# Optimization experiments

Measured on AMD Instinct MI355X. Metric: run time of the kernel, lower is better.

The kernel has to match this reference:

```python
import jax, jax.numpy as jnp
import numpy as np

B, T, C, H, N = 2, 1024, 2048, 32, 64  # batch, seq, n_embd==dim_att, heads, head_size
EPS_GN = 64e-5  # torch GroupNorm eps=0.00064


def setup_inputs() -> dict:
    key = jax.random.key(0)
    ks = jax.random.split(key, 40)
    def rn(i, shape, s):
        return jax.random.normal(ks[i], shape, dtype=jnp.float32) * s
    return {
        'x': jax.random.normal(ks[0], (B, T, C), dtype=jnp.float32),
        'shift_state': jnp.zeros((B, C), jnp.float32),
        'wkv_state': jnp.zeros((B, H, N, N), jnp.float32),
        'time_maa_x': rn(1, (1, 1, C), 0.3),
        'time_maa_rg': rn(2, (1, 1, C), 0.3),
        'time_maa_wa': rn(3, (1, 1, C), 0.3),
        'time_maa_k': rn(4, (1, 1, C), 0.3),
        'time_maa_v': rn(5, (1, 1, C), 0.3),
        'time_maa_w1': rn(6, (C, 128), 0.02),   # D_MIX_LORA*4 = 128
        'time_maa_w2': rn(7, (4, 32, C), 0.02),
        'time_decay': rn(8, (1, 1, C), 0.5) - 4.0,
        'time_decay_w1': rn(9, (C, 64), 0.02),
        'time_decay_w2': rn(10, (64, C), 0.02),
        'time_faaaa': rn(11, (1, 1, H, N), 0.02),
        'time_aaaaa': rn(12, (1, 1, C), 0.02),
        'time_aaa_w1': rn(13, (C, 16), 0.02),
        'time_aaa_w2': rn(14, (16, C), 0.02),
        'time_kkk_w1': rn(15, (C, 16), 0.02),
        'time_kkk_w2': rn(16, (16, C), 0.02),
        'gate_w1': rn(17, (C, 128), 0.02),
        'gate_w2': rn(18, (128, C), 0.02),
        'ma_w1': rn(19, (C, 16), 0.02),
        'ma_w2': rn(20, (16, C), 0.02),
        'time_misc_a': rn(21, (1, 1, C), 0.02),
        'mk_w1': rn(22, (C, 16), 0.02),
        'mk_w2': rn(23, (16, C), 0.02),
        'time_misc_k': rn(24, (1, 1, C), 0.02),
        'Wr': rn(25, (C, C), 0.5 / np.sqrt(C)),
        'Wk': rn(26, (C, C), 0.05 / np.sqrt(C)),
        'Wv': rn(27, (C, C), 0.5 / np.sqrt(C)),
        'Wo': rn(28, (C, C), 0.5 / np.sqrt(C)),
        'ln_w': jnp.ones((C,), jnp.float32),
        'ln_b': jnp.zeros((C,), jnp.float32),
    }


def _forward(x, shift_state, wkv_state, time_maa_x, time_maa_rg, time_maa_wa,
             time_maa_k, time_maa_v, time_maa_w1, time_maa_w2, time_decay,
             time_decay_w1, time_decay_w2, time_faaaa, time_aaaaa, time_aaa_w1,
             time_aaa_w2, time_kkk_w1, time_kkk_w2, gate_w1, gate_w2, ma_w1,
             ma_w2, time_misc_a, mk_w1, mk_w2, time_misc_k, Wr, Wk, Wv, Wo,
             ln_w, ln_b):
    # token shift difference
    xx = jnp.concatenate([shift_state[:, None, :], x[:, :-1]], axis=1) - x
    xmx = x + xx * time_maa_x
    m = jnp.tanh(xmx @ time_maa_w1).reshape(B, T, 4, -1)   # [B,T,4,32]
    m = jnp.einsum('btfd,fdc->fbtc', m, time_maa_w2)       # [4,B,T,C]
    mrg, mwa, mkm, mv = m[0], m[1], m[2], m[3]
    xrg = x + xx * (time_maa_rg + mrg)
    xwa = x + xx * (time_maa_wa + mwa)
    xk = x + xx * (time_maa_k + mkm)
    xv = x + xx * (time_maa_v + mv)
    r = xrg @ Wr.T
    w = -jax.nn.softplus(-(time_decay + jnp.tanh(xwa @ time_decay_w1) @ time_decay_w2)) - 0.5
    k = xk @ Wk.T
    v = xv @ Wv.T
    g = jnp.tanh(xrg @ gate_w1) @ gate_w2
    kk = k + jnp.tanh(xk @ time_kkk_w1) @ time_kkk_w2
    kkh = kk.reshape(B, T, H, N)
    nrm = jnp.maximum(jnp.linalg.norm(kkh, axis=-1, keepdims=True), 1e-12)  # F.normalize
    kk = (kkh / nrm).reshape(B, T, C)
    a = jax.nn.sigmoid(time_aaaaa + xwa @ time_aaa_w1 @ time_aaa_w2)
    ma = jax.nn.sigmoid(time_misc_a + xwa @ ma_w1 @ ma_w2)
    k = k * ma + k * a * (1.0 - ma)
    mk = jax.nn.sigmoid(time_misc_k + xk @ mk_w1 @ mk_w2)
    k = k * jnp.exp(jnp.minimum(w * mk, 0.0))  # clamp(w*mk, max=0).exp()

    # RWKV-7 recurrence (fused_recurrent_rwkv7 with a=-kk, b=kk*a_gate):
    #   S_t = diag(exp(w_t)) S_{t-1} + b_t (a_t^T S_{t-1}) + k_t v_t^T,  o_t = S_t^T r_t
    def heads(t):
        return jnp.moveaxis(t.reshape(B, T, H, N), 1, 0)  # [T,B,H,N]
    rs, ksq, vs, ws = heads(r), heads(k), heads(v), heads(w)
    a_s, b_s = heads(-kk), heads(kk * a)

    def step(S, inputs):  # S: [B,H,N_key,N_val]
        r_t, k_t, v_t, w_t, a_t, b_t = inputs
        sa = jnp.einsum('bhk,bhkv->bhv', a_t, S)
        S = S * jnp.exp(w_t)[..., None] + k_t[..., None] * v_t[..., None, :] + b_t[..., None] * sa[..., None, :]
        o = jnp.einsum('bhk,bhkv->bhv', r_t, S)
        return S, o

    S_final, o = jax.lax.scan(step, wkv_state, (rs, ksq, vs, ws, a_s, b_s))
    out = jnp.moveaxis(o, 0, 1).reshape(B, T, C)

    # GroupNorm(n_head groups, eps=64e-5), biased variance per head
    y = out.reshape(B * T, H, N)
    mu = y.mean(-1, keepdims=True)
    var = ((y - mu) ** 2).mean(-1, keepdims=True)
    y = (y - mu) / jnp.sqrt(var + EPS_GN)
    y = y * ln_w.reshape(H, N) + ln_b.reshape(H, N)
    xo = y.reshape(B, T, C)

    rh = r.reshape(B, T, H, N)
    kh = k.reshape(B, T, H, N)
    vh = v.reshape(B, T, H, N)
    xo = xo + ((rh * kh * time_faaaa).sum(-1, keepdims=True) * vh).reshape(B, T, C)
    xo = (xo * g) @ Wo.T
    return xo, x[:, -1], S_final


def reference(x, shift_state, wkv_state, time_maa_x, time_maa_rg, time_maa_wa,
              time_maa_k, time_maa_v, time_maa_w1, time_maa_w2, time_decay,
              time_decay_w1, time_decay_w2, time_faaaa, time_aaaaa, time_aaa_w1,
              time_aaa_w2, time_kkk_w1, time_kkk_w2, gate_w1, gate_w2, ma_w1,
              ma_w2, time_misc_a, mk_w1, mk_w2, time_misc_k, Wr, Wk, Wv, Wo,
              ln_w, ln_b):
    return _forward(x, shift_state, wkv_state, time_maa_x, time_maa_rg, time_maa_wa,
                    time_maa_k, time_maa_v, time_maa_w1, time_maa_w2, time_decay,
                    time_decay_w1, time_decay_w2, time_faaaa, time_aaaaa, time_aaa_w1,
                    time_aaa_w2, time_kkk_w1, time_kkk_w2, gate_w1, gate_w2, ma_w1,
                    ma_w2, time_misc_a, mk_w1, mk_w2, time_misc_k, Wr, Wk, Wv, Wo,
                    ln_w, ln_b)
```

## Files before the change

### kernel.cpp

```cpp
#include <hip/hip_runtime.h>
#include <hip/hip_bf16.h>
#include <math.h>


#define B_ 2
#define T_ 1024
#define C_ 2048
#define H_ 32
#define BT_ (B_*T_)
#define BTC_ ((size_t)BT_*C_)
#define CC_ ((size_t)C_*C_)
#define KS_ 8
#define CH_ 8

typedef __bf16 bf16x8 __attribute__((ext_vector_type(8)));
typedef float f32x4 __attribute__((ext_vector_type(4)));

__device__ __forceinline__ float wave64_sum(float v){
#pragma unroll
  for (int d = 1; d < 64; d <<= 1) v += __shfl_xor(v, d, 64);
  return v;
}

__device__ __forceinline__ float dpp_add_xor1(float x){
  int j = __builtin_amdgcn_mov_dpp(__float_as_int(x), 0xB1, 0xF, 0xF, true);
  return x + __int_as_float(j);
}
__device__ __forceinline__ float dpp_add_xor2(float x){
  int j = __builtin_amdgcn_mov_dpp(__float_as_int(x), 0x4E, 0xF, 0xF, true);
  return x + __int_as_float(j);
}
__device__ __forceinline__ float dpp_add_hmir(float x){
  int j = __builtin_amdgcn_mov_dpp(__float_as_int(x), 0x141, 0xF, 0xF, true);
  return x + __int_as_float(j);
}
__device__ __forceinline__ float dpp_add_mir(float x){
  int j = __builtin_amdgcn_mov_dpp(__float_as_int(x), 0x140, 0xF, 0xF, true);
  return x + __int_as_float(j);
}

__device__ __forceinline__ float red16(float x){
  x = dpp_add_xor1(x);
  x = dpp_add_xor2(x);
  x = dpp_add_hmir(x);
  x = dpp_add_mir(x);
  return x;
}

__device__ __forceinline__ size_t bhtn_idx(int r, int c){
  return (((size_t)(r >> 10)*H_ + (c >> 6))*T_ + (r & 1023))*64 + (c & 63);
}

__device__ __forceinline__ void gload_lds16(const float* g, float* l){
  __builtin_amdgcn_global_load_lds((const __attribute__((address_space(1))) void*)g,
                                   (__attribute__((address_space(3))) void*)l, 16, 0, 0);
}
__device__ __forceinline__ void gload_lds16b(const __hip_bfloat16* g, __bf16* l){
  __builtin_amdgcn_global_load_lds((const __attribute__((address_space(1))) void*)g,
                                   (__attribute__((address_space(3))) void*)l, 16, 0, 0);
}

__global__ __launch_bounds__(256) void f2bf_kernel(const float* __restrict__ in,
                                                   __hip_bfloat16* __restrict__ out, size_t n){
  size_t i = (size_t)blockIdx.x*256 + threadIdx.x;
  if (i < n) out[i] = __float2bfloat16(in[i]);
}

__global__ __launch_bounds__(256) void shift_kernel(const float* __restrict__ x,
                                                    const float* __restrict__ shift,
                                                    const float* __restrict__ maa_x,
                                                    float* __restrict__ xx, __hip_bfloat16* __restrict__ xmx_h){
  size_t idx = (size_t)blockIdx.x*256 + threadIdx.x;
  int c = (int)(idx % C_);
  size_t bt = idx / C_;
  int t = (int)(bt % T_);
  int b = (int)(bt / T_);
  float xv = x[idx];
  float prev = (t == 0) ? shift[(size_t)b*C_ + c] : x[idx - C_];
  float d = prev - xv;
  xx[idx] = d;
  xmx_h[idx] = __float2bfloat16(xv + d * maa_x[c]);
}

__global__ __launch_bounds__(256) void tp_pack(const float* __restrict__ in, __hip_bfloat16* __restrict__ out,
                                               int Nsrc, int row_off){
  __shared__ float tile[32][33];
  const int t = threadIdx.x;
  const int k0 = blockIdx.x*32, n0 = blockIdx.y*32;
  const int tn = t & 31, tk = t >> 5;
#pragma unroll
  for (int q = 0; q < 4; q++){
    int ki = tk + 8*q;
    float v = (n0 + tn < Nsrc) ? in[(size_t)(k0+ki)*Nsrc + n0 + tn] : 0.f;
    tile[tn][ki] = v;
  }
  __syncthreads();
#pragma unroll
  for (int q = 0; q < 4; q++){
    int no = tk + 8*q;
    if (n0 + no < Nsrc)
      out[(size_t)(row_off + n0 + no)*2048 + k0 + tn] = __float2bfloat16(tile[no][tn]);
  }
}

__global__ __launch_bounds__(256) void gemm_sk(const __hip_bfloat16* __restrict__ Ah,
                                               const __hip_bfloat16* __restrict__ Bh,
                                               float* __restrict__ parts, int K, int KC){
  __shared__ __bf16 As[2][128*32];
  __shared__ __bf16 Bs[2][128*32];
  const int tid = threadIdx.x;
  const int bm = blockIdx.x*128;
  const int z = blockIdx.y;
  const int wid = tid >> 6, lane = tid & 63;
  const int wr = (wid >> 1)*64, wc = (wid & 1)*64;
  const int fr = lane & 15, kg = lane >> 4;
  const int srow = tid >> 2, sk = (tid & 3)*8;
  f32x4 acc[4][4] = {};
  const int kend = z*KC + KC;
#define SK_STAGE(kt_, b_) do{ \
    gload_lds16b(Ah + (size_t)(bm+srow)*K + (kt_) + sk,    As[b_] + wid*512); \
    gload_lds16b(Ah + (size_t)(bm+srow+64)*K + (kt_) + sk, As[b_] + wid*512 + 64*32); \
    gload_lds16b(Bh + (size_t)(srow)*K + (kt_) + sk,       Bs[b_] + wid*512); \
    gload_lds16b(Bh + (size_t)(srow+64)*K + (kt_) + sk,    Bs[b_] + wid*512 + 64*32); \
  }while(0)
  SK_STAGE(z*KC, 0);
  __builtin_amdgcn_s_waitcnt(0x3F70);
  __builtin_amdgcn_s_barrier();
  __builtin_amdgcn_sched_barrier(0);
  int buf = 0;
  for (int kt = z*KC; kt < kend; kt += 32){
    if (kt + 32 < kend) SK_STAGE(kt+32, buf^1);
    bf16x8 af[4], bfr[4];
#pragma unroll
    for (int i = 0; i < 4; i++){
      af[i]  = *(const bf16x8*)(As[buf] + (wr + i*16 + fr)*32 + kg*8);
      bfr[i] = *(const bf16x8*)(Bs[buf] + (wc + i*16 + fr)*32 + kg*8);
    }
#pragma unroll
    for (int mi = 0; mi < 4; mi++)
#pragma unroll
      for (int ni = 0; ni < 4; ni++)
        acc[mi][ni] = __builtin_amdgcn_mfma_f32_16x16x32_bf16(af[mi], bfr[ni], acc[mi][ni], 0, 0, 0);
    __builtin_amdgcn_sched_barrier(0);
    __builtin_amdgcn_s_waitcnt(0x3F70);
    __builtin_amdgcn_s_barrier();
    __builtin_amdgcn_sched_barrier(0);
    buf ^= 1;
  }
#undef SK_STAGE
  float* Cc = parts + (size_t)z*BT_*128;
  const int orow0 = bm + wr + kg*4;
  const int ocol0 = wc + fr;
#pragma unroll
  for (int mi = 0; mi < 4; mi++)
#pragma unroll
    for (int ni = 0; ni < 4; ni++)
#pragma unroll
      for (int j = 0; j < 4; j++)
        Cc[(size_t)(orow0 + mi*16 + j)*128 + ocol0 + ni*16] = acc[mi][ni][j];
}

__global__ __launch_bounds__(256) void reduce_sk(const float* __restrict__ parts, float* __restrict__ out,
                                                 int tanh_lo, int tanh_hi){
  size_t idx = (size_t)blockIdx.x*256 + threadIdx.x;
  float s = 0.f;
#pragma unroll
  for (int z = 0; z < KS_; z++) s += parts[(size_t)z*BT_*128 + idx];
  int c = (int)(idx & 127);
  if (c >= tanh_lo && c < tanh_hi) s = tanhf(s);
  out[idx] = s;
}

__global__ __launch_bounds__(256) void mm_sk_g(const float* __restrict__ A, const float* __restrict__ W,
                                               __hip_bfloat16* __restrict__ out, int K){
  const int j = blockIdx.y*256 + threadIdx.x;
  const int i0 = blockIdx.x*8;
  float acc[8] = {0,0,0,0,0,0,0,0};
  for (int k = 0; k < K; k++){
    float wv = W[(size_t)k*C_ + j];
#pragma unroll
    for (int r = 0; r < 8; r++) acc[r] += A[(size_t)(i0+r)*K + k] * wv;
  }
#pragma unroll
  for (int r = 0; r < 8; r++) out[(size_t)(i0+r)*C_ + j] = __float2bfloat16(acc[r]);
}

__global__ __launch_bounds__(256) void mix_kernel(
    const float* __restrict__ m1, const float* __restrict__ w2,
    const float* __restrict__ x, const float* __restrict__ xx,
    const float* __restrict__ maa_rg, const float* __restrict__ maa_wa,
    const float* __restrict__ maa_k, const float* __restrict__ maa_v,
    __hip_bfloat16* __restrict__ xrg_h, __hip_bfloat16* __restrict__ xwa_h,
    __hip_bfloat16* __restrict__ xk_h, __hip_bfloat16* __restrict__ xv_h)
{
  const int j = blockIdx.y*256 + threadIdx.x;
  const int i0 = blockIdx.x*8;
  float acc[4][8] = {};
#pragma unroll
  for (int f = 0; f < 4; f++){
    for (int d = 0; d < 32; d++){
      float wv = w2[((size_t)f*32 + d)*C_ + j];
#pragma unroll
      for (int r = 0; r < 8; r++)
        acc[f][r] += m1[(size_t)(i0+r)*128 + f*32 + d] * wv;
    }
  }
  float mrg_ = maa_rg[j], mwa_ = maa_wa[j], mk_ = maa_k[j], mv_ = maa_v[j];
#pragma unroll
  for (int r = 0; r < 8; r++){
    size_t idx = (size_t)(i0+r)*C_ + j;
    float xval = x[idx], xxv = xx[idx];
    xrg_h[idx] = __float2bfloat16(xval + xxv*(mrg_ + acc[0][r]));
    xwa_h[idx] = __float2bfloat16(xval + xxv*(mwa_ + acc[1][r]));
    xk_h[idx]  = __float2bfloat16(xval + xxv*(mk_  + acc[2][r]));
    xv_h[idx]  = __float2bfloat16(xval + xxv*(mv_  + acc[3][r]));
  }
}

__global__ __launch_bounds__(256) void gemm_bt(const __hip_bfloat16* __restrict__ Ah,
                                               const __hip_bfloat16* __restrict__ Bh,
                                               float* __restrict__ Cc, int M, int Nn, int K){
  __shared__ __bf16 As[2][128*32];
  __shared__ __bf16 Bs[2][128*32];
  const int tid = threadIdx.x;
  const int bm = blockIdx.x*128, bn = blockIdx.y*128;
  const int wid = tid >> 6, lane = tid & 63;
  const int wr = (wid >> 1)*64, wc = (wid & 1)*64;
  const int fr = lane & 15, kg = lane >> 4;
  const int srow = tid >> 2, sk = (tid & 3)*8;
  f32x4 acc[4][4] = {};
#define BT_STAGE(kt_, b_) do{ \
    gload_lds16b(Ah + (size_t)(bm+srow)*K + (kt_) + sk,    As[b_] + wid*512); \
    gload_lds16b(Ah + (size_t)(bm+srow+64)*K + (kt_) + sk, As[b_] + wid*512 + 64*32); \
    gload_lds16b(Bh + (size_t)(bn+srow)*K + (kt_) + sk,    Bs[b_] + wid*512); \
    gload_lds16b(Bh + (size_t)(bn+srow+64)*K + (kt_) + sk, Bs[b_] + wid*512 + 64*32); \
  }while(0)
  BT_STAGE(0, 0);
  __builtin_amdgcn_s_waitcnt(0x3F70);
  __builtin_amdgcn_s_barrier();
  __builtin_amdgcn_sched_barrier(0);
  int buf = 0;
  for (int kt = 0; kt < K; kt += 32){
    if (kt + 32 < K) BT_STAGE(kt+32, buf^1);
    bf16x8 af[4], bfr[4];
#pragma unroll
    for (int i = 0; i < 4; i++){
      af[i]  = *(const bf16x8*)(As[buf] + (wr + i*16 + fr)*32 + kg*8);
      bfr[i] = *(const bf16x8*)(Bs[buf] + (wc + i*16 + fr)*32 + kg*8);
    }
#pragma unroll
    for (int mi = 0; mi < 4; mi++)
#pragma unroll
      for (int ni = 0; ni < 4; ni++)
        acc[mi][ni] = __builtin_amdgcn_mfma_f32_16x16x32_bf16(af[mi], bfr[ni], acc[mi][ni], 0, 0, 0);
    __builtin_amdgcn_sched_barrier(0);
    __builtin_amdgcn_s_waitcnt(0x3F70);
    __builtin_amdgcn_s_barrier();
    __builtin_amdgcn_sched_barrier(0);
    buf ^= 1;
  }
#undef BT_STAGE
  const int orow0 = bm + wr + kg*4;
  const int ocol0 = bn + wc + fr;
#pragma unroll
  for (int mi = 0; mi < 4; mi++)
#pragma unroll
    for (int ni = 0; ni < 4; ni++)
#pragma unroll
      for (int j = 0; j < 4; j++)
        Cc[(size_t)(orow0 + mi*16 + j)*Nn + ocol0 + ni*16] = acc[mi][ni][j];
}

__global__ __launch_bounds__(256) void gemm_bt_T3(
    const __hip_bfloat16* __restrict__ A0, const __hip_bfloat16* __restrict__ A1,
    const __hip_bfloat16* __restrict__ A2,
    const __hip_bfloat16* __restrict__ B0, const __hip_bfloat16* __restrict__ B1,
    const __hip_bfloat16* __restrict__ B2,
    float* __restrict__ C0, float* __restrict__ C1, float* __restrict__ C2, int K)
{
  __shared__ __bf16 As[2][128*32];
  __shared__ __bf16 Bs[2][128*32];
  const int zi = blockIdx.z;
  const __hip_bfloat16* Ah = (zi == 0) ? A0 : (zi == 1) ? A1 : A2;
  const __hip_bfloat16* Bh = (zi == 0) ? B0 : (zi == 1) ? B1 : B2;
  float* Cc = (zi == 0) ? C0 : (zi == 1) ? C1 : C2;
  const int tid = threadIdx.x;
  const int bm = blockIdx.x*128, bn = blockIdx.y*128;
  const int wid = tid >> 6, lane = tid & 63;
  const int wr = (wid >> 1)*64, wc = (wid & 1)*64;
  const int fr = lane & 15, kg = lane >> 4;
  const int srow = tid >> 2, sk = (tid & 3)*8;
  f32x4 acc[4][4] = {};
#define T3_STAGE(kt_, b_) do{ \
    gload_lds16b(Ah + (size_t)(bm+srow)*K + (kt_) + sk,    As[b_] + wid*512); \
    gload_lds16b(Ah + (size_t)(bm+srow+64)*K + (kt_) + sk, As[b_] + wid*512 + 64*32); \
    gload_lds16b(Bh + (size_t)(bn+srow)*K + (kt_) + sk,    Bs[b_] + wid*512); \
    gload_lds16b(Bh + (size_t)(bn+srow+64)*K + (kt_) + sk, Bs[b_] + wid*512 + 64*32); \
  }while(0)
  T3_STAGE(0, 0);
  __builtin_amdgcn_s_waitcnt(0x3F70);
  __builtin_amdgcn_s_barrier();
  __builtin_amdgcn_sched_barrier(0);
  int buf = 0;
  for (int kt = 0; kt < K; kt += 32){
    if (kt + 32 < K) T3_STAGE(kt+32, buf^1);
    bf16x8 af[4], bfr[4];
#pragma unroll
    for (int i = 0; i < 4; i++){
      af[i]  = *(const bf16x8*)(As[buf] + (wr + i*16 + fr)*32 + kg*8);
      bfr[i] = *(const bf16x8*)(Bs[buf] + (wc + i*16 + fr)*32 + kg*8);
    }
#pragma unroll
    for (int mi = 0; mi < 4; mi++)
#pragma unroll
      for (int ni = 0; ni < 4; ni++)
        acc[mi][ni] = __builtin_amdgcn_mfma_f32_16x16x32_bf16(af[mi], bfr[ni], acc[mi][ni], 0, 0, 0);
    __builtin_amdgcn_sched_barrier(0);
    __builtin_amdgcn_s_waitcnt(0x3F70);
    __builtin_amdgcn_s_barrier();
    __builtin_amdgcn_sched_barrier(0);
    buf ^= 1;
  }
#undef T3_STAGE
  const int r0 = bm + wr + kg*4;
  const int c0 = bn + wc + fr;
#pragma unroll
  for (int mi = 0; mi < 4; mi++)
#pragma unroll
    for (int ni = 0; ni < 4; ni++)
#pragma unroll
      for (int j = 0; j < 4; j++)
        Cc[bhtn_idx(r0 + mi*16 + j, c0 + ni*16)] = acc[mi][ni][j];
}

__global__ __launch_bounds__(256) void lora2_kernel(
    const float* __restrict__ wa1, const float* __restrict__ k1c,
    const float* __restrict__ dw2, const float* __restrict__ aw2, const float* __restrict__ maw2,
    const float* __restrict__ mkw2, const float* __restrict__ kkw2,
    const float* __restrict__ td, const float* __restrict__ aaaaa,
    const float* __restrict__ misc_a, const float* __restrict__ misc_k,
    float* __restrict__ k0, float* __restrict__ a_out,
    float* __restrict__ ew_out, float* __restrict__ kk0_out)
{
  const int j = blockIdx.y*256 + threadIdx.x;
  const int i0 = blockIdx.x*8;
  float accW[8] = {}, accA[8] = {}, accMA[8] = {}, accMK[8] = {}, accKK[8] = {};
  for (int k = 0; k < 64; k++){
    float wv = dw2[(size_t)k*C_ + j];
#pragma unroll
    for (int r = 0; r < 8; r++) accW[r] += wa1[(size_t)(i0+r)*128 + k] * wv;
  }
  for (int k = 0; k < 16; k++){
    float w_a  = aw2[(size_t)k*C_ + j];
    float w_ma = maw2[(size_t)k*C_ + j];
    float w_mk = mkw2[(size_t)k*C_ + j];
    float w_kk = kkw2[(size_t)k*C_ + j];
#pragma unroll
    for (int r = 0; r < 8; r++){
      accA[r]  += wa1[(size_t)(i0+r)*128 + 64 + k] * w_a;
      accMA[r] += wa1[(size_t)(i0+r)*128 + 80 + k] * w_ma;
      accKK[r] += k1c[(size_t)(i0+r)*128 + k] * w_kk;
      accMK[r] += k1c[(size_t)(i0+r)*128 + 16 + k] * w_mk;
    }
  }
  float tdv = td[j], aav = aaaaa[j], mav = misc_a[j], mkv = misc_k[j];
#pragma unroll
  for (int r = 0; r < 8; r++){
    size_t idx = bhtn_idx(i0+r, j);
    float u  = tdv + accW[r];
    float w  = -log1pf(expf(-u)) - 0.5f;
    float a  = 1.f/(1.f + expf(-(aav + accA[r])));
    float ma = 1.f/(1.f + expf(-(mav + accMA[r])));
    float mk = 1.f/(1.f + expf(-(mkv + accMK[r])));
    float kv = k0[idx];
    kk0_out[idx] = kv + accKK[r];
    float kn = kv * (ma + a*(1.f - ma)) * expf(fminf(w*mk, 0.f));
    k0[idx] = kn;
    a_out[idx] = a;
    ew_out[idx] = expf(w);
  }
}

__global__ __launch_bounds__(256) void kknorm_kernel(float* __restrict__ kk0, float* __restrict__ a_bs){
  const size_t grp = (size_t)blockIdx.x*4 + (threadIdx.x >> 6);
  const int lane = threadIdx.x & 63;
  const size_t idx = grp*64 + lane;
  float kv = kk0[idx];
  float ss = wave64_sum(kv*kv);
  float nrm = fmaxf(sqrtf(ss), 1e-12f);
  float kkn = kv / nrm;
  kk0[idx] = kkn;
  a_bs[idx] = kkn * a_bs[idx];
}

__global__ __launch_bounds__(64, 1) void rec_kernel(
    const float* __restrict__ rr, const float* __restrict__ kx,
    const float* __restrict__ vx, const float* __restrict__ ew,
    const float* __restrict__ kkv, const float* __restrict__ bsv,
    const float* __restrict__ s0, float* __restrict__ o, float* __restrict__ sT)
{
  __shared__ __align__(16) float lds[2][6][CH_*64];
  const int g = blockIdx.x;
  const int bh = g & 63;
  const int vg = g >> 6;
  const int b = bh >> 5, h = bh & 31;
  const int lane = threadIdx.x;
  const int cf = lane >> 4;
  const int kq = lane & 15;
  const int k0 = kq*4;
  const int v = vg*4 + cf;

  float S0, S1, S2, S3;
  {
    const float* p = s0 + ((size_t)bh*64 + k0)*64 + v;
    S0 = p[0]; S1 = p[64]; S2 = p[128]; S3 = p[192];
  }

  const size_t sb = (size_t)bh*T_*64;
  const float* g0 = kkv + sb;
  const float* g1 = ew  + sb;
  const float* g2 = kx  + sb;
  const float* g3 = bsv + sb;
  const float* g4 = rr  + sb;
  const float* g5 = vx  + sb;
  float* ob = o + (size_t)b*T_*C_ + h*64 + v;

#define STAGE(c, buf) do{ \
    const size_t co_ = (size_t)(c)*(CH_*64) + lane*4; \
    _Pragma("unroll") \
    for (int j_ = 0; j_ < 2; j_++){ \
      gload_lds16(g0 + co_ + j_*256, &lds[buf][0][j_*256]); \
      gload_lds16(g1 + co_ + j_*256, &lds[buf][1][j_*256]); \
      gload_lds16(g2 + co_ + j_*256, &lds[buf][2][j_*256]); \
      gload_lds16(g3 + co_ + j_*256, &lds[buf][3][j_*256]); \
      gload_lds16(g4 + co_ + j_*256, &lds[buf][4][j_*256]); \
      gload_lds16(g5 + co_ + j_*256, &lds[buf][5][j_*256]); \
    } }while(0)

  STAGE(0, 0);
  const int NCH = T_/CH_;
  for (int c = 0; c < NCH; c++){
    const int cn = (c+1 < NCH) ? c+1 : c;
    STAGE(cn, (c+1)&1);
    __builtin_amdgcn_s_waitcnt(0x0F7C);
    __builtin_amdgcn_sched_barrier(0);
    const int buf = c & 1;
#pragma unroll
    for (int s = 0; s < CH_; s++){
      const int so = s*64 + k0;
      const float4 A  = *(const float4*)(&lds[buf][0][so]);
      const float4 E  = *(const float4*)(&lds[buf][1][so]);
      const float4 Kk = *(const float4*)(&lds[buf][2][so]);
      const float4 Bv = *(const float4*)(&lds[buf][3][so]);
      const float4 R  = *(const float4*)(&lds[buf][4][so]);
      const float vt  = lds[buf][5][s*64 + v];
      float p = (A.x*S0 + A.y*S1) + (A.z*S2 + A.w*S3);
      p = red16(p);
      S0 = S0*E.x + Kk.x*vt - Bv.x*p;
      S1 = S1*E.y + Kk.y*vt - Bv.y*p;
      S2 = S2*E.z + Kk.z*vt - Bv.z*p;
      S3 = S3*E.w + Kk.w*vt - Bv.w*p;
      float op = (R.x*S0 + R.y*S1) + (R.z*S2 + R.w*S3);
      op = red16(op);
      if (kq == 0)
        ob[(size_t)(c*CH_ + s)*C_] = op;
    }
  }
#undef STAGE
  float* pT = sT + ((size_t)bh*64 + k0)*64 + v;
  pT[0] = S0; pT[64] = S1; pT[128] = S2; pT[192] = S3;
}

__global__ __launch_bounds__(256) void post_kernel(
    const float* __restrict__ o, const float* __restrict__ r, const float* __restrict__ k,
    const float* __restrict__ v, const __hip_bfloat16* __restrict__ g,
    const float* __restrict__ lnw, const float* __restrict__ lnb,
    const float* __restrict__ faaaa, __hip_bfloat16* __restrict__ z_h)
{
  const size_t grp = (size_t)blockIdx.x*4 + (threadIdx.x >> 6);
  const int lane = threadIdx.x & 63;
  const int h = (int)(grp & (H_-1));
  const int bt = (int)(grp >> 5);
  const size_t idx  = grp*64 + lane;
  const size_t idx2 = (((size_t)(bt >> 10)*H_ + h)*T_ + (bt & 1023))*64 + lane;
  const int ci = h*64 + lane;
  float y = o[idx];
  float mu = wave64_sum(y) * (1.f/64.f);
  float d = y - mu;
  float var = wave64_sum(d*d) * (1.f/64.f);
  float yn = d * rsqrtf(var + 64e-5f) * lnw[ci] + lnb[ci];
  float s = wave64_sum(r[idx2]*k[idx2]*faaaa[ci]);
  float xo = yn + s*v[idx2];
  z_h[idx] = __float2bfloat16(xo * __bfloat162float(g[idx]));
}

__global__ __launch_bounds__(256) void lastx_kernel(const float* __restrict__ x, float* __restrict__ out1){
  int idx = blockIdx.x*256 + threadIdx.x;
  int b = idx / C_, c = idx % C_;
  out1[idx] = x[((size_t)b*T_ + (T_-1))*C_ + c];
}

extern "C" void kernel_launch(void* const* d_in, const int* in_sizes, int n_in,
                              void* d_out, int out_size, void* d_ws, size_t ws_size,
                              hipStream_t stream){
  (void)in_sizes; (void)n_in; (void)out_size;
  const float* x      = (const float*)d_in[0];
  const float* shift  = (const float*)d_in[1];
  const float* wkv0   = (const float*)d_in[2];
  const float* maa_x  = (const float*)d_in[3];
  const float* maa_rg = (const float*)d_in[4];
  const float* maa_wa = (const float*)d_in[5];
  const float* maa_k  = (const float*)d_in[6];
  const float* maa_v  = (const float*)d_in[7];
  const float* maa_w1 = (const float*)d_in[8];
  const float* maa_w2 = (const float*)d_in[9];
  const float* tdecay = (const float*)d_in[10];
  const float* dw1    = (const float*)d_in[11];
  const float* dw2    = (const float*)d_in[12];
  const float* faaaa  = (const float*)d_in[13];
  const float* aaaaa  = (const float*)d_in[14];
  const float* aw1    = (const float*)d_in[15];
  const float* aw2    = (const float*)d_in[16];
  const float* kkw1   = (const float*)d_in[17];
  const float* kkw2   = (const float*)d_in[18];
  const float* gw1    = (const float*)d_in[19];
  const float* gw2    = (const float*)d_in[20];
  const float* maw1   = (const float*)d_in[21];
  const float* maw2   = (const float*)d_in[22];
  const float* misc_a = (const float*)d_in[23];
  const float* mkw1   = (const float*)d_in[24];
  const float* mkw2   = (const float*)d_in[25];
  const float* misc_k = (const float*)d_in[26];
  const float* Wr     = (const float*)d_in[27];
  const float* Wk     = (const float*)d_in[28];
  const float* Wv     = (const float*)d_in[29];
  const float* Wo     = (const float*)d_in[30];
  const float* lnw    = (const float*)d_in[31];
  const float* lnb    = (const float*)d_in[32];

  float* out0 = (float*)d_out;
  float* out1 = out0 + BTC_;
  float* outS = out1 + (size_t)B_*C_;

  const size_t NEEDED = (6*BTC_ + (size_t)3*BT_*128)*4 + 5*CC_*2 + (size_t)4*128*2048*2;
  if (ws_size < NEEDED) return;

  float* ws = (float*)d_ws;
  float* rbuf  = ws;
  float* kbuf  = ws + 1*BTC_;
  float* vbuf  = ws + 2*BTC_;
  float* abuf  = ws + 3*BTC_;
  float* ewbuf = ws + 4*BTC_;
  float* kkbuf = ws + 5*BTC_;
  float* xx    = abuf;
  float* wa1   = ws + 6*BTC_;
  float* g1f   = wa1 + (size_t)BT_*128;
  float* k1c   = g1f + (size_t)BT_*128;
  float* parts = rbuf;
  float* m1f   = vbuf;
  __hip_bfloat16* hb = (__hip_bfloat16*)(k1c + (size_t)BT_*128);
  __hip_bfloat16* xrg_h = hb;
  __hip_bfloat16* xwa_h = hb + 1*CC_;
  __hip_bfloat16* xk_h  = hb + 2*CC_;
  __hip_bfloat16* xv_h  = hb + 3*CC_;
  __hip_bfloat16* Wb    = hb + 4*CC_;
  __hip_bfloat16* WtB   = hb + 5*CC_;
  __hip_bfloat16* Wt_m  = WtB;
  __hip_bfloat16* Wt_wa = WtB + (size_t)128*2048;
  __hip_bfloat16* Wt_g  = WtB + (size_t)2*128*2048;
  __hip_bfloat16* Wt_k  = WtB + (size_t)3*128*2048;
  __hip_bfloat16* xmx_h = xv_h;
  __hip_bfloat16* g_h   = xwa_h;
  __hip_bfloat16* z_h   = xv_h;
  __hip_bfloat16* Wk_h  = (__hip_bfloat16*)ewbuf;
  __hip_bfloat16* Wv_h  = (__hip_bfloat16*)kkbuf;

  dim3 blk(256);
  const int KC = C_/KS_;

  hipMemsetAsync(WtB, 0, (size_t)4*128*2048*2, stream);
  tp_pack<<<dim3(64,4), blk, 0, stream>>>(maa_w1, Wt_m, 128, 0);
  tp_pack<<<dim3(64,2), blk, 0, stream>>>(dw1,  Wt_wa, 64, 0);
  tp_pack<<<dim3(64,1), blk, 0, stream>>>(aw1,  Wt_wa, 16, 64);
  tp_pack<<<dim3(64,1), blk, 0, stream>>>(maw1, Wt_wa, 16, 80);
  tp_pack<<<dim3(64,4), blk, 0, stream>>>(gw1,  Wt_g, 128, 0);
  tp_pack<<<dim3(64,1), blk, 0, stream>>>(kkw1, Wt_k, 16, 0);
  tp_pack<<<dim3(64,1), blk, 0, stream>>>(mkw1, Wt_k, 16, 16);

  shift_kernel<<<(int)(BTC_/256), blk, 0, stream>>>(x, shift, maa_x, xx, xmx_h);

  gemm_sk<<<dim3(BT_/128, KS_), blk, 0, stream>>>(xmx_h, Wt_m, parts, C_, KC);
  reduce_sk<<<BT_*128/256, blk, 0, stream>>>(parts, m1f, 0, 128);

  mix_kernel<<<dim3(BT_/8, C_/256), blk, 0, stream>>>(m1f, maa_w2, x, xx, maa_rg, maa_wa, maa_k, maa_v,
                                                      xrg_h, xwa_h, xk_h, xv_h);
  gemm_sk<<<dim3(BT_/128, KS_), blk, 0, stream>>>(xwa_h, Wt_wa, parts, C_, KC);
  reduce_sk<<<BT_*128/256, blk, 0, stream>>>(parts, wa1, 0, 64);
  gemm_sk<<<dim3(BT_/128, KS_), blk, 0, stream>>>(xrg_h, Wt_g, parts, C_, KC);
  reduce_sk<<<BT_*128/256, blk, 0, stream>>>(parts, g1f, 0, 128);
  gemm_sk<<<dim3(BT_/128, KS_), blk, 0, stream>>>(xk_h, Wt_k, parts, C_, KC);
  reduce_sk<<<BT_*128/256, blk, 0, stream>>>(parts, k1c, 0, 16);

  mm_sk_g<<<dim3(BT_/8, C_/256), blk, 0, stream>>>(g1f, gw2, g_h, 128);

  f2bf_kernel<<<(int)(CC_/256), blk, 0, stream>>>(Wr, Wb, CC_);
  f2bf_kernel<<<(int)(CC_/256), blk, 0, stream>>>(Wk, Wk_h, CC_);
  f2bf_kernel<<<(int)(CC_/256), blk, 0, stream>>>(Wv, Wv_h, CC_);
  gemm_bt_T3<<<dim3(BT_/128, C_/128, 3), blk, 0, stream>>>(xrg_h, xk_h, xv_h,
                                                           Wb, Wk_h, Wv_h,
                                                           rbuf, kbuf, vbuf, C_);

  lora2_kernel<<<dim3(BT_/8, C_/256), blk, 0, stream>>>(wa1, k1c,
                                                        dw2, aw2, maw2, mkw2, kkw2,
                                                        tdecay, aaaaa, misc_a, misc_k,
                                                        kbuf, abuf, ewbuf, kkbuf);
  kknorm_kernel<<<BT_*H_/4, blk, 0, stream>>>(kkbuf, abuf);

  rec_kernel<<<1024, dim3(64), 0, stream>>>(rbuf, kbuf, vbuf, ewbuf, kkbuf, abuf, wkv0, out0, outS);

  post_kernel<<<BT_*H_/4, blk, 0, stream>>>(out0, rbuf, kbuf, vbuf, g_h, lnw, lnb, faaaa, z_h);
  f2bf_kernel<<<(int)(CC_/256), blk, 0, stream>>>(Wo, Wb, CC_);
  gemm_bt<<<dim3(BT_/128, C_/128), blk, 0, stream>>>(z_h, Wb, out0, BT_, C_, C_);
  lastx_kernel<<<(B_*C_)/256, blk, 0, stream>>>(x, out1);
}
```

Measured before the change: 771.9 us.

## Batch the three LoRA split-K GEMMs, merge weight casts, fuse kk-normalization into lora2

The three small split-K GEMMs (wa, gate, k LoRA first stages) become one launch indexed by blockIdx.z, and their three reductions become one. They use rbuf/kbuf/vbuf as separate partial-sum scratch so the GEMMs can run concurrently. The three fp32-to-bf16 weight casts are merged into one launch. The per-head L2 normalization of kk and the kk*a product move into lora2_kernel via a wave-wide reduction, since a 64-lane wave covers one head. This removes a separate kknorm pass over two BTC buffers. The goal is fewer launches, better CU occupancy for the small 128-block GEMMs, and less global memory traffic. The cost is reusing the r/k/v buffers as scratch before they are written.

```diff
diff --git a/kernel.cpp b/kernel.cpp
--- a/kernel.cpp
+++ b/kernel.cpp
@@ -64,6 +64,17 @@
                                                    __hip_bfloat16* __restrict__ out, size_t n){
   size_t i = (size_t)blockIdx.x*256 + threadIdx.x;
   if (i < n) out[i] = __float2bfloat16(in[i]);
+}
+
+__global__ __launch_bounds__(256) void f2bf3_kernel(const float* __restrict__ i0, const float* __restrict__ i1,
+                                                    const float* __restrict__ i2,
+                                                    __hip_bfloat16* __restrict__ o0, __hip_bfloat16* __restrict__ o1,
+                                                    __hip_bfloat16* __restrict__ o2){
+  const int z = blockIdx.y;
+  const float* in = (z == 0) ? i0 : (z == 1) ? i1 : i2;
+  __hip_bfloat16* out = (z == 0) ? o0 : (z == 1) ? o1 : o2;
+  size_t i = (size_t)blockIdx.x*256 + threadIdx.x;
+  if (i < CC_) out[i] = __float2bfloat16(in[i]);
 }
 
 __global__ __launch_bounds__(256) void shift_kernel(const float* __restrict__ x,
@@ -160,6 +171,71 @@
         Cc[(size_t)(orow0 + mi*16 + j)*128 + ocol0 + ni*16] = acc[mi][ni][j];
 }
 
+__global__ __launch_bounds__(256) void gemm_sk3(
+    const __hip_bfloat16* __restrict__ A0, const __hip_bfloat16* __restrict__ A1,
+    const __hip_bfloat16* __restrict__ A2,
+    const __hip_bfloat16* __restrict__ B0, const __hip_bfloat16* __restrict__ B1,
+    const __hip_bfloat16* __restrict__ B2,
+    float* __restrict__ P0, float* __restrict__ P1, float* __restrict__ P2, int K, int KC)
+{
+  __shared__ __bf16 As[2][128*32];
+  __shared__ __bf16 Bs[2][128*32];
+  const int zi = blockIdx.z;
+  const __hip_bfloat16* Ah = (zi == 0) ? A0 : (zi == 1) ? A1 : A2;
+  const __hip_bfloat16* Bh = (zi == 0) ? B0 : (zi == 1) ? B1 : B2;
+  float* parts = (zi == 0) ? P0 : (zi == 1) ? P1 : P2;
+  const int tid = threadIdx.x;
+  const int bm = blockIdx.x*128;
+  const int z = blockIdx.y;
+  const int wid = tid >> 6, lane = tid & 63;
+  const int wr = (wid >> 1)*64, wc = (wid & 1)*64;
+  const int fr = lane & 15, kg = lane >> 4;
+  const int srow = tid >> 2, sk = (tid & 3)*8;
+  f32x4 acc[4][4] = {};
+  const int kend = z*KC + KC;
+#define SK3_STAGE(kt_, b_) do{ \
+    gload_lds16b(Ah + (size_t)(bm+srow)*K + (kt_) + sk,    As[b_] + wid*512); \
+    gload_lds16b(Ah + (size_t)(bm+srow+64)*K + (kt_) + sk, As[b_] + wid*512 + 64*32); \
+    gload_lds16b(Bh + (size_t)(srow)*K + (kt_) + sk,       Bs[b_] + wid*512); \
+    gload_lds16b(Bh + (size_t)(srow+64)*K + (kt_) + sk,    Bs[b_] + wid*512 + 64*32); \
+  }while(0)
+  SK3_STAGE(z*KC, 0);
+  __builtin_amdgcn_s_waitcnt(0x3F70);
+  __builtin_amdgcn_s_barrier();
+  __builtin_amdgcn_sched_barrier(0);
+  int buf = 0;
+  for (int kt = z*KC; kt < kend; kt += 32){
+    if (kt + 32 < kend) SK3_STAGE(kt+32, buf^1);
+    bf16x8 af[4], bfr[4];
+#pragma unroll
+    for (int i = 0; i < 4; i++){
+      af[i]  = *(const bf16x8*)(As[buf] + (wr + i*16 + fr)*32 + kg*8);
+      bfr[i] = *(const bf16x8*)(Bs[buf] + (wc + i*16 + fr)*32 + kg*8);
+    }
+#pragma unroll
+    for (int mi = 0; mi < 4; mi++)
+#pragma unroll
+      for (int ni = 0; ni < 4; ni++)
+        acc[mi][ni] = __builtin_amdgcn_mfma_f32_16x16x32_bf16(af[mi], bfr[ni], acc[mi][ni], 0, 0, 0);
+    __builtin_amdgcn_sched_barrier(0);
+    __builtin_amdgcn_s_waitcnt(0x3F70);
+    __builtin_amdgcn_s_barrier();
+    __builtin_amdgcn_sched_barrier(0);
+    buf ^= 1;
+  }
+#undef SK3_STAGE
+  float* Cc = parts + (size_t)z*BT_*128;
+  const int orow0 = bm + wr + kg*4;
+  const int ocol0 = wc + fr;
+#pragma unroll
+  for (int mi = 0; mi < 4; mi++)
+#pragma unroll
+    for (int ni = 0; ni < 4; ni++)
+#pragma unroll
+      for (int j = 0; j < 4; j++)
+        Cc[(size_t)(orow0 + mi*16 + j)*128 + ocol0 + ni*16] = acc[mi][ni][j];
+}
+
 __global__ __launch_bounds__(256) void reduce_sk(const float* __restrict__ parts, float* __restrict__ out,
                                                  int tanh_lo, int tanh_hi){
   size_t idx = (size_t)blockIdx.x*256 + threadIdx.x;
@@ -168,6 +244,23 @@
   for (int z = 0; z < KS_; z++) s += parts[(size_t)z*BT_*128 + idx];
   int c = (int)(idx & 127);
   if (c >= tanh_lo && c < tanh_hi) s = tanhf(s);
+  out[idx] = s;
+}
+
+__global__ __launch_bounds__(256) void reduce_sk3(const float* __restrict__ P0, const float* __restrict__ P1,
+                                                  const float* __restrict__ P2,
+                                                  float* __restrict__ O0, float* __restrict__ O1,
+                                                  float* __restrict__ O2){
+  const int zi = blockIdx.y;
+  const float* parts = (zi == 0) ? P0 : (zi == 1) ? P1 : P2;
+  float* out = (zi == 0) ? O0 : (zi == 1) ? O1 : O2;
+  const int hi = (zi == 0) ? 64 : (zi == 1) ? 128 : 16;
+  size_t idx = (size_t)blockIdx.x*256 + threadIdx.x;
+  float s = 0.f;
+#pragma unroll
+  for (int z = 0; z < KS_; z++) s += parts[(size_t)z*BT_*128 + idx];
+  int c = (int)(idx & 127);
+  if (c < hi) s = tanhf(s);
   out[idx] = s;
 }
 
@@ -339,7 +432,7 @@
     const float* __restrict__ mkw2, const float* __restrict__ kkw2,
     const float* __restrict__ td, const float* __restrict__ aaaaa,
     const float* __restrict__ misc_a, const float* __restrict__ misc_k,
-    float* __restrict__ k0, float* __restrict__ a_out,
+    float* __restrict__ k0, float* __restrict__ b_out,
     float* __restrict__ ew_out, float* __restrict__ kk0_out)
 {
   const int j = blockIdx.y*256 + threadIdx.x;
@@ -373,24 +466,15 @@
     float ma = 1.f/(1.f + expf(-(mav + accMA[r])));
     float mk = 1.f/(1.f + expf(-(mkv + accMK[r])));
     float kv = k0[idx];
-    kk0_out[idx] = kv + accKK[r];
+    float kk = kv + accKK[r];
+    float ss  = wave64_sum(kk*kk);
+    float kkn = kk / fmaxf(sqrtf(ss), 1e-12f);
+    kk0_out[idx] = kkn;
+    b_out[idx]   = kkn * a;
     float kn = kv * (ma + a*(1.f - ma)) * expf(fminf(w*mk, 0.f));
     k0[idx] = kn;
-    a_out[idx] = a;
     ew_out[idx] = expf(w);
   }
-}
-
-__global__ __launch_bounds__(256) void kknorm_kernel(float* __restrict__ kk0, float* __restrict__ a_bs){
-  const size_t grp = (size_t)blockIdx.x*4 + (threadIdx.x >> 6);
-  const int lane = threadIdx.x & 63;
-  const size_t idx = grp*64 + lane;
-  float kv = kk0[idx];
-  float ss = wave64_sum(kv*kv);
-  float nrm = fmaxf(sqrtf(ss), 1e-12f);
-  float kkn = kv / nrm;
-  kk0[idx] = kkn;
-  a_bs[idx] = kkn * a_bs[idx];
 }
 
 __global__ __launch_bounds__(64, 1) void rec_kernel(
@@ -594,18 +678,15 @@
 
   mix_kernel<<<dim3(BT_/8, C_/256), blk, 0, stream>>>(m1f, maa_w2, x, xx, maa_rg, maa_wa, maa_k, maa_v,
                                                       xrg_h, xwa_h, xk_h, xv_h);
-  gemm_sk<<<dim3(BT_/128, KS_), blk, 0, stream>>>(xwa_h, Wt_wa, parts, C_, KC);
-  reduce_sk<<<BT_*128/256, blk, 0, stream>>>(parts, wa1, 0, 64);
-  gemm_sk<<<dim3(BT_/128, KS_), blk, 0, stream>>>(xrg_h, Wt_g, parts, C_, KC);
-  reduce_sk<<<BT_*128/256, blk, 0, stream>>>(parts, g1f, 0, 128);
-  gemm_sk<<<dim3(BT_/128, KS_), blk, 0, stream>>>(xk_h, Wt_k, parts, C_, KC);
-  reduce_sk<<<BT_*128/256, blk, 0, stream>>>(parts, k1c, 0, 16);
+
+  gemm_sk3<<<dim3(BT_/128, KS_, 3), blk, 0, stream>>>(xwa_h, xrg_h, xk_h,
+                                                      Wt_wa, Wt_g, Wt_k,
+                                                      rbuf, kbuf, vbuf, C_, KC);
+  reduce_sk3<<<dim3(BT_*128/256, 3), blk, 0, stream>>>(rbuf, kbuf, vbuf, wa1, g1f, k1c);
 
   mm_sk_g<<<dim3(BT_/8, C_/256), blk, 0, stream>>>(g1f, gw2, g_h, 128);
 
-  f2bf_kernel<<<(int)(CC_/256), blk, 0, stream>>>(Wr, Wb, CC_);
-  f2bf_kernel<<<(int)(CC_/256), blk, 0, stream>>>(Wk, Wk_h, CC_);
-  f2bf_kernel<<<(int)(CC_/256), blk, 0, stream>>>(Wv, Wv_h, CC_);
+  f2bf3_kernel<<<dim3((int)(CC_/256), 3), blk, 0, stream>>>(Wr, Wk, Wv, Wb, Wk_h, Wv_h);
   gemm_bt_T3<<<dim3(BT_/128, C_/128, 3), blk, 0, stream>>>(xrg_h, xk_h, xv_h,
                                                            Wb, Wk_h, Wv_h,
                                                            rbuf, kbuf, vbuf, C_);
@@ -614,7 +695,6 @@
                                                         dw2, aw2, maw2, mkw2, kkw2,
                                                         tdecay, aaaaa, misc_a, misc_k,
                                                         kbuf, abuf, ewbuf, kkbuf);
-  kknorm_kernel<<<BT_*H_/4, blk, 0, stream>>>(kkbuf, abuf);
 
   rec_kernel<<<1024, dim3(64), 0, stream>>>(rbuf, kbuf, vbuf, ewbuf, kkbuf, abuf, wkv0, out0, outS);
 
```

Result: faster. 736.0 us (-4.7%).
